# Kernel tuning notes

Hardware: AMD Instinct MI355X
Metric: run time of the kernel (lower is better)

Reference implementation:

```python
import jax, jax.numpy as jnp
import numpy as np

B, TH, TS, HS, WS = 16, 1024, 1024, 1024, 1024


def setup_inputs() -> dict:
    key = jax.random.key(0)
    k1, k2, k3, k4 = jax.random.split(key, 4)
    h = jax.random.normal(k1, (B, TH, HS), dtype=jnp.float32)
    s = jax.random.normal(k2, (B, TS, WS), dtype=jnp.float32)
    # nn.Linear params: weight [out, in], bias [out]
    Wh = jax.random.normal(k3, (HS, HS), dtype=jnp.float32) * 0.02
    bh = jnp.zeros((HS,), dtype=jnp.float32)
    Ws = jax.random.normal(k4, (HS, WS), dtype=jnp.float32) * 0.02
    bs = jnp.zeros((HS,), dtype=jnp.float32)
    return {"h": h, "s": s, "Wh": Wh, "bh": bh, "Ws": Ws, "bs": bs}


def reference(h, s, Wh, bh, Ws, bs):
    hp = jnp.einsum('bth,oh->bto', h, Wh) + bh          # [B, TH, HS]
    sp = jnp.einsum('btw,ow->bto', s, Ws) + bs          # [B, TS, HS]
    scores = jnp.einsum('bik,bjk->bij', hp, sp)         # [B, TH, TS]
    b, th, _ = scores.shape
    # faithful to torch: flat-chunk into rows of length TH, softmax over dim 1
    sm = jax.nn.softmax(scores.reshape(-1, th), axis=1).reshape(b, -1, th)  # [B, TS, TH]
    res = jnp.matmul(sm, hp)                            # [B, TS, HS]
    return res.reshape(-1, res.shape[-1])               # [B*TS, HS]
```

## Files before the change

kernel.cpp:

```cpp
#include <hip/hip_runtime.h>
#include <hip/hip_bf16.h>
#include <stdint.h>


typedef _Float16 half_t;
typedef __attribute__((ext_vector_type(8))) _Float16 half8;
typedef __attribute__((ext_vector_type(4))) _Float16 half4;
typedef __attribute__((ext_vector_type(4))) float floatx4;

__device__ __forceinline__ void gl2lds16(const void* g, void* l) {
    __builtin_amdgcn_global_load_lds(
        (const __attribute__((address_space(1))) uint32_t*)(uintptr_t)g,
        (__attribute__((address_space(3))) uint32_t*)(uintptr_t)l,
        16, 0, 0);
}

#define PH_MID() do { \
    asm volatile("s_barrier\n\ts_waitcnt lgkmcnt(0)" ::: "memory"); \
    __builtin_amdgcn_sched_barrier(0); } while (0)

#define PH_END() asm volatile("s_barrier" ::: "memory")

#define QUAD(mq, nq) do { \
    __builtin_amdgcn_s_setprio(1); \
    _Pragma("unroll") for (int mi = 0; mi < 4; ++mi) \
    _Pragma("unroll") for (int ni = 0; ni < 2; ++ni) \
    _Pragma("unroll") for (int ks = 0; ks < 2; ++ks) \
        acc[(mq)*4+mi][(nq)*2+ni] = __builtin_amdgcn_mfma_f32_16x16x32_f16( \
            aF[mi][ks], bF[nq][ni][ks], acc[(mq)*4+mi][(nq)*2+ni], 0, 0, 0); \
    __builtin_amdgcn_s_setprio(0); } while (0)

#define NT16 16

template<int WF32, int WH16, int WH16T>
__global__ __launch_bounds__(512, 2) void gemm256(
    const half_t* __restrict__ A, const half_t* __restrict__ B,
    const float* __restrict__ bias,
    float* __restrict__ Cf, half_t* __restrict__ Ch, half_t* __restrict__ ChT,
    int lda, int ldb, int N,
    long aBatch, long bBatch, long cfBatch, int ldcf)
{
    extern __shared__ char smem[];

    const int tid  = threadIdx.x;
    const int wave = tid >> 6;
    const int lane = tid & 63;
    const int wr = wave >> 2;
    const int wc = wave & 3;
    const int lr = lane & 15, lg = lane >> 4;

    const long batch = blockIdx.z;
    const half_t* Ab = A + batch * aBatch;
    const half_t* Bb = B + batch * bBatch;
    const int row0 = blockIdx.x * 256;
    const int col0 = blockIdx.y * 256;

    floatx4 acc[8][4];
#pragma unroll
    for (int m = 0; m < 8; ++m)
#pragma unroll
        for (int n = 0; n < 4; ++n)
            acc[m][n] = (floatx4){0.f, 0.f, 0.f, 0.f};

    long aOff[2][2], bOff[2][2];
#pragma unroll
    for (int hh = 0; hh < 2; ++hh)
#pragma unroll
        for (int i = 0; i < 2; ++i) {
            const int off = hh * 16384 + i * 8192 + tid * 16;
            const int e = off ^ (((off >> 7) & 7) << 4);
            const int r = e >> 7, cb = e & 127;
            aOff[hh][i] = (long)(row0 + r) * (long)(lda * 2) + cb;
            bOff[hh][i] = (long)(col0 + r) * (long)(ldb * 2) + cb;
        }

    const int wave_s = __builtin_amdgcn_readfirstlane(wave);
    auto stageHalf = [&](int buf, int isA, int hh, int kk) {
#pragma unroll
        for (int i = 0; i < 2; ++i) {
            const char* g = (isA ? (const char*)Ab + aOff[hh][i]
                                 : (const char*)Bb + bOff[hh][i]) + (long)kk * 2;
            gl2lds16(g, smem + buf * 65536 + (isA ? 0 : 32768)
                          + hh * 16384 + i * 8192 + wave_s * 1024);
        }
    };

    uint32_t aof0 = (uint32_t)((wr * 128 + lr) * 128 + ((lg * 16) ^ ((lr & 7) << 4)));
    uint32_t aof1 = (uint32_t)((wr * 128 + lr) * 128 + ((64 + lg * 16) ^ ((lr & 7) << 4)));
    uint32_t bof0 = (uint32_t)(32768 + (wc * 64 + lr) * 128 + ((lg * 16) ^ ((lr & 7) << 4)));
    uint32_t bof1 = (uint32_t)(32768 + (wc * 64 + lr) * 128 + ((64 + lg * 16) ^ ((lr & 7) << 4)));

    stageHalf(0, 0, 0, 0);   stageHalf(0, 0, 1, 0);
    stageHalf(0, 1, 0, 0);   stageHalf(0, 1, 1, 0);
    stageHalf(1, 0, 0, 64);  stageHalf(1, 0, 1, 64);
    asm volatile("s_waitcnt vmcnt(4)" ::: "memory");
    asm volatile("s_barrier" ::: "memory");

    half8 aF[4][2];
    half8 bF[2][2][2];

    for (int t = 0; t < NT16; ++t) {
#pragma unroll
        for (int mi = 0; mi < 4; ++mi) {
            aF[mi][0] = *(const half8*)(smem + aof0 + mi * 2048);
            aF[mi][1] = *(const half8*)(smem + aof1 + mi * 2048);
        }
#pragma unroll
        for (int ni = 0; ni < 2; ++ni) {
            bF[0][ni][0] = *(const half8*)(smem + bof0 + ni * 2048);
            bF[0][ni][1] = *(const half8*)(smem + bof1 + ni * 2048);
        }
        if (t + 1 < NT16) stageHalf((t & 1) ^ 1, 1, 0, (t + 1) * 64);
        PH_MID();
        QUAD(0, 0);
        PH_END();

#pragma unroll
        for (int ni = 0; ni < 2; ++ni) {
            bF[1][ni][0] = *(const half8*)(smem + bof0 + (2 + ni) * 2048);
            bF[1][ni][1] = *(const half8*)(smem + bof1 + (2 + ni) * 2048);
        }
        if (t + 1 < NT16) stageHalf((t & 1) ^ 1, 1, 1, (t + 1) * 64);
        PH_MID();
        QUAD(0, 1);
        PH_END();

#pragma unroll
        for (int mi = 0; mi < 4; ++mi) {
            aF[mi][0] = *(const half8*)(smem + aof0 + (4 + mi) * 2048);
            aF[mi][1] = *(const half8*)(smem + aof1 + (4 + mi) * 2048);
        }
        if (t + 2 < NT16) stageHalf(t & 1, 0, 0, (t + 2) * 64);
        PH_MID();
        QUAD(1, 1);
        PH_END();

        if (t + 2 < NT16) {
            stageHalf(t & 1, 0, 1, (t + 2) * 64);
            asm volatile("s_waitcnt vmcnt(4)" ::: "memory");
        } else {
            asm volatile("s_waitcnt vmcnt(0)" ::: "memory");
        }
        PH_MID();
        QUAD(1, 0);
        PH_END();

        aof0 ^= 65536; aof1 ^= 65536; bof0 ^= 65536; bof1 ^= 65536;
    }

    {
        float* wlds = (float*)(smem + wave * 2304);
        float bv[4];
#pragma unroll
        for (int n = 0; n < 4; ++n)
            bv[n] = bias ? bias[col0 + wc * 64 + n * 16 + lr] : 0.f;
        const int er = lane >> 2, ec = lane & 3;
        const int oc = lane >> 1, tc = lane & 1;
#pragma unroll
        for (int m = 0; m < 8; ++m) {
#pragma unroll
            for (int np = 0; np < 2; ++np) {
#pragma unroll
                for (int n2 = 0; n2 < 2; ++n2)
#pragma unroll
                    for (int j = 0; j < 4; ++j)
                        wlds[(lg * 4 + j) * 36 + n2 * 16 + lr] =
                            acc[m][np * 2 + n2][j] + bv[np * 2 + n2];
                const int grow = row0 + wr * 128 + m * 16;
                const int gcol = col0 + wc * 64 + np * 32;
                float4 q0 = *(float4*)&wlds[er * 36 + ec * 8];
                float4 q1 = *(float4*)&wlds[er * 36 + ec * 8 + 4];
                if (WF32) {
                    float* p = Cf + batch * cfBatch + (long)(grow + er) * ldcf + gcol + ec * 8;
                    *(float4*)p = q0;
                    *(float4*)(p + 4) = q1;
                }
                if (WH16) {
                    half8 o = { (half_t)q0.x, (half_t)q0.y, (half_t)q0.z, (half_t)q0.w,
                                (half_t)q1.x, (half_t)q1.y, (half_t)q1.z, (half_t)q1.w };
                    *(half8*)&Ch[(long)(grow + er) * N + gcol + ec * 8] = o;
                }
                if (WH16T) {
                    float tv[8];
#pragma unroll
                    for (int k = 0; k < 8; ++k)
                        tv[k] = wlds[(tc * 8 + k) * 36 + oc];
                    half8 o = { (half_t)tv[0], (half_t)tv[1], (half_t)tv[2], (half_t)tv[3],
                                (half_t)tv[4], (half_t)tv[5], (half_t)tv[6], (half_t)tv[7] };
                    const int gt = grow + tc * 8;
                    *(half8*)&ChT[(long)(gt >> 10) * 1048576
                                  + (long)(gcol + oc) * 1024 + (gt & 1023)] = o;
                }
                __builtin_amdgcn_s_waitcnt(0);
            }
        }
    }
}

__global__ void softmax_inplace(float* __restrict__ S) {
    const long r = blockIdx.x;
    float* row = S + r * 1024;
    const int tid = threadIdx.x;
    const int wave = tid >> 6, lane = tid & 63;

    float4 v = ((const float4*)row)[tid];
    float mx = fmaxf(fmaxf(v.x, v.y), fmaxf(v.z, v.w));
#pragma unroll
    for (int off = 32; off > 0; off >>= 1)
        mx = fmaxf(mx, __shfl_xor(mx, off));
    __shared__ float rmx[4], rsm[4];
    if (lane == 0) rmx[wave] = mx;
    __syncthreads();
    mx = fmaxf(fmaxf(rmx[0], rmx[1]), fmaxf(rmx[2], rmx[3]));

    float e0 = __expf(v.x - mx), e1 = __expf(v.y - mx);
    float e2 = __expf(v.z - mx), e3 = __expf(v.w - mx);
    float s = e0 + e1 + e2 + e3;
#pragma unroll
    for (int off = 32; off > 0; off >>= 1)
        s += __shfl_xor(s, off);
    if (lane == 0) rsm[wave] = s;
    __syncthreads();
    s = rsm[0] + rsm[1] + rsm[2] + rsm[3];

    const float inv = 1.0f / s;
    half4 o = { (half_t)(e0 * inv), (half_t)(e1 * inv), (half_t)(e2 * inv), (half_t)(e3 * inv) };
    ((half4*)((half_t*)S + r * 2048))[tid] = o;
}

__global__ void cvt_f16(const float4* __restrict__ src, half4* __restrict__ dst, int n4) {
    const int stride = gridDim.x * blockDim.x;
    for (int i = blockIdx.x * blockDim.x + threadIdx.x; i < n4; i += stride) {
        float4 v = src[i];
        half4 o = { (half_t)v.x, (half_t)v.y, (half_t)v.z, (half_t)v.w };
        dst[i] = o;
    }
}

extern "C" void kernel_launch(void* const* d_in, const int* in_sizes, int n_in,
                              void* d_out, int out_size, void* d_ws, size_t ws_size,
                              hipStream_t stream) {
    const float* h  = (const float*)d_in[0];
    const float* s  = (const float*)d_in[1];
    const float* Wh = (const float*)d_in[2];
    const float* bh = (const float*)d_in[3];
    const float* Ws = (const float*)d_in[4];
    const float* bs = (const float*)d_in[5];

    const long MB = 16384;
    const long D  = 1024;

    char* w = (char*)d_ws;
    half_t* h16 = (half_t*)w;  w += MB * D * 2;
    half_t* s16 = (half_t*)w;  w += MB * D * 2;
    float*  sc  = (float*)h16;
    half_t* Wh16 = (half_t*)w;  w += D * D * 2;
    half_t* Ws16 = (half_t*)w;  w += D * D * 2;
    half_t* hp16 = (half_t*)w;  w += MB * D * 2;
    half_t* sp16 = (half_t*)w;  w += MB * D * 2;
    half_t* hpT  = (half_t*)w;  w += MB * D * 2;

    hipFuncSetAttribute(reinterpret_cast<const void*>(&gemm256<0,1,1>),
                        hipFuncAttributeMaxDynamicSharedMemorySize, 131072);
    hipFuncSetAttribute(reinterpret_cast<const void*>(&gemm256<0,1,0>),
                        hipFuncAttributeMaxDynamicSharedMemorySize, 131072);
    hipFuncSetAttribute(reinterpret_cast<const void*>(&gemm256<1,0,0>),
                        hipFuncAttributeMaxDynamicSharedMemorySize, 131072);

    cvt_f16<<<512,  256, 0, stream>>>((const float4*)Wh, (half4*)Wh16, (int)(D * D / 4));
    cvt_f16<<<512,  256, 0, stream>>>((const float4*)Ws, (half4*)Ws16, (int)(D * D / 4));
    cvt_f16<<<2048, 256, 0, stream>>>((const float4*)h,  (half4*)h16,  (int)(MB * D / 4));
    cvt_f16<<<2048, 256, 0, stream>>>((const float4*)s,  (half4*)s16,  (int)(MB * D / 4));

    gemm256<0,1,1><<<dim3(64, 4, 1), 512, 131072, stream>>>(
        h16, Wh16, bh, nullptr, hp16, hpT, 1024, 1024, 1024, 0, 0, 0, 0);
    gemm256<0,1,0><<<dim3(64, 4, 1), 512, 131072, stream>>>(
        s16, Ws16, bs, nullptr, sp16, nullptr, 1024, 1024, 1024, 0, 0, 0, 0);
    gemm256<1,0,0><<<dim3(4, 4, 16), 512, 131072, stream>>>(
        hp16, sp16, nullptr, sc, nullptr, nullptr, 1024, 1024, 1024,
        1048576L, 1048576L, 1048576L, 1024);
    softmax_inplace<<<16384, 256, 0, stream>>>(sc);
    gemm256<1,0,0><<<dim3(4, 4, 16), 512, 131072, stream>>>(
        (const half_t*)sc, hpT, nullptr, (float*)d_out, nullptr, nullptr,
        2048, 1024, 1024, 2097152L, 1048576L, 1048576L, 1024);
}
```

Measured before the change: 238.7 us.

## Replace four-phase ping-pong GEMM schedule with simple double-buffered loop

Drops the hand-tuned four-quadrant schedule, which used explicit barriers, setprio and staggered partial stage loads with vmcnt waits. In its place is a plain double-buffered loop: each iteration issues every load for the next K tile up front, computes two half-M blocks from LDS, and ends with one __syncthreads. This cuts barrier count and code complexity but loses the fine-grained overlap of loads with MFMA. It also relies on __syncthreads to drain the global-to-LDS loads, with no explicit vmcnt wait.

```diff
diff --git a/kernel.cpp b/kernel.cpp
--- a/kernel.cpp
+++ b/kernel.cpp
@@ -14,21 +14,6 @@
         (__attribute__((address_space(3))) uint32_t*)(uintptr_t)l,
         16, 0, 0);
 }
-
-#define PH_MID() do { \
-    asm volatile("s_barrier\n\ts_waitcnt lgkmcnt(0)" ::: "memory"); \
-    __builtin_amdgcn_sched_barrier(0); } while (0)
-
-#define PH_END() asm volatile("s_barrier" ::: "memory")
-
-#define QUAD(mq, nq) do { \
-    __builtin_amdgcn_s_setprio(1); \
-    _Pragma("unroll") for (int mi = 0; mi < 4; ++mi) \
-    _Pragma("unroll") for (int ni = 0; ni < 2; ++ni) \
-    _Pragma("unroll") for (int ks = 0; ks < 2; ++ks) \
-        acc[(mq)*4+mi][(nq)*2+ni] = __builtin_amdgcn_mfma_f32_16x16x32_f16( \
-            aF[mi][ks], bF[nq][ni][ks], acc[(mq)*4+mi][(nq)*2+ni], 0, 0, 0); \
-    __builtin_amdgcn_s_setprio(0); } while (0)
 
 #define NT16 16
 
@@ -90,61 +75,52 @@
     uint32_t bof0 = (uint32_t)(32768 + (wc * 64 + lr) * 128 + ((lg * 16) ^ ((lr & 7) << 4)));
     uint32_t bof1 = (uint32_t)(32768 + (wc * 64 + lr) * 128 + ((64 + lg * 16) ^ ((lr & 7) << 4)));
 
-    stageHalf(0, 0, 0, 0);   stageHalf(0, 0, 1, 0);
-    stageHalf(0, 1, 0, 0);   stageHalf(0, 1, 1, 0);
-    stageHalf(1, 0, 0, 64);  stageHalf(1, 0, 1, 64);
-    asm volatile("s_waitcnt vmcnt(4)" ::: "memory");
-    asm volatile("s_barrier" ::: "memory");
-
-    half8 aF[4][2];
-    half8 bF[2][2][2];
+    stageHalf(0, 1, 0, 0);  stageHalf(0, 1, 1, 0);
+    stageHalf(0, 0, 0, 0);  stageHalf(0, 0, 1, 0);
+    __syncthreads();
 
     for (int t = 0; t < NT16; ++t) {
+        if (t + 1 < NT16) {
+            const int nxt = (t & 1) ^ 1;
+            const int k1 = (t + 1) * 64;
+            stageHalf(nxt, 1, 0, k1);  stageHalf(nxt, 1, 1, k1);
+            stageHalf(nxt, 0, 0, k1);  stageHalf(nxt, 0, 1, k1);
+        }
+
+        half8 aF[4][2], bF[4][2];
+#pragma unroll
+        for (int ni = 0; ni < 4; ++ni) {
+            bF[ni][0] = *(const half8*)(smem + bof0 + ni * 2048);
+            bF[ni][1] = *(const half8*)(smem + bof1 + ni * 2048);
+        }
 #pragma unroll
         for (int mi = 0; mi < 4; ++mi) {
             aF[mi][0] = *(const half8*)(smem + aof0 + mi * 2048);
             aF[mi][1] = *(const half8*)(smem + aof1 + mi * 2048);
         }
 #pragma unroll
-        for (int ni = 0; ni < 2; ++ni) {
-            bF[0][ni][0] = *(const half8*)(smem + bof0 + ni * 2048);
-            bF[0][ni][1] = *(const half8*)(smem + bof1 + ni * 2048);
-        }
-        if (t + 1 < NT16) stageHalf((t & 1) ^ 1, 1, 0, (t + 1) * 64);
-        PH_MID();
-        QUAD(0, 0);
-        PH_END();
-
-#pragma unroll
-        for (int ni = 0; ni < 2; ++ni) {
-            bF[1][ni][0] = *(const half8*)(smem + bof0 + (2 + ni) * 2048);
-            bF[1][ni][1] = *(const half8*)(smem + bof1 + (2 + ni) * 2048);
-        }
-        if (t + 1 < NT16) stageHalf((t & 1) ^ 1, 1, 1, (t + 1) * 64);
-        PH_MID();
-        QUAD(0, 1);
-        PH_END();
-
+        for (int mi = 0; mi < 4; ++mi)
+#pragma unroll
+            for (int ni = 0; ni < 4; ++ni)
+#pragma unroll
+                for (int ks = 0; ks < 2; ++ks)
+                    acc[mi][ni] = __builtin_amdgcn_mfma_f32_16x16x32_f16(
+                        aF[mi][ks], bF[ni][ks], acc[mi][ni], 0, 0, 0);
 #pragma unroll
         for (int mi = 0; mi < 4; ++mi) {
             aF[mi][0] = *(const half8*)(smem + aof0 + (4 + mi) * 2048);
             aF[mi][1] = *(const half8*)(smem + aof1 + (4 + mi) * 2048);
         }
-        if (t + 2 < NT16) stageHalf(t & 1, 0, 0, (t + 2) * 64);
-        PH_MID();
-        QUAD(1, 1);
-        PH_END();
-
-        if (t + 2 < NT16) {
-            stageHalf(t & 1, 0, 1, (t + 2) * 64);
-            asm volatile("s_waitcnt vmcnt(4)" ::: "memory");
-        } else {
-            asm volatile("s_waitcnt vmcnt(0)" ::: "memory");
-        }
-        PH_MID();
-        QUAD(1, 0);
-        PH_END();
-
+#pragma unroll
+        for (int mi = 0; mi < 4; ++mi)
+#pragma unroll
+            for (int ni = 0; ni < 4; ++ni)
+#pragma unroll
+                for (int ks = 0; ks < 2; ++ks)
+                    acc[4 + mi][ni] = __builtin_amdgcn_mfma_f32_16x16x32_f16(
+                        aF[mi][ks], bF[ni][ks], acc[4 + mi][ni], 0, 0, 0);
+
+        __syncthreads();
         aof0 ^= 65536; aof1 ^= 65536; bof0 ^= 65536; bof1 ^= 65536;
     }
 
```

Result: no change. 236.8 us (-0.8%).
